# Kernel optimization log

Hardware: AMD Instinct MI355X
Metric: run time of the kernel (lower is better)

Reference implementation:

```python
import jax, jax.numpy as jnp
import numpy as np

N, C, G = 262144, 256, 1024
R = C // 4  # reduction bottleneck


def _linear_w(key, out_dim, in_dim):
    # torch.nn.Linear default init: U(-1/sqrt(in), 1/sqrt(in)), weight shape [out, in]
    bound = 1.0 / np.sqrt(in_dim)
    return jax.random.uniform(key, (out_dim, in_dim), jnp.float32, -bound, bound)


def setup_inputs() -> dict:
    key = jax.random.key(0)
    ks = jax.random.split(key, 8)
    return {
        "x": jax.random.normal(ks[0], (N, C), jnp.float32),
        "glb_w1": _linear_w(ks[1], R, C),
        "glb_a": jnp.full((1,), 0.25, jnp.float32),   # PReLU param (default init 0.25)
        "glb_w2": _linear_w(ks[2], C, R),
        "local_w1": _linear_w(ks[3], R, C),
        "local_a": jnp.full((1,), 0.25, jnp.float32),
        "local_w2": _linear_w(ks[4], C, R),
        "attn_w1": _linear_w(ks[5], R, C),
        "attn_a": jnp.full((1,), 0.25, jnp.float32),
        "attn_w2": _linear_w(ks[6], C, R),
        "batch_idx": jnp.sort(jax.random.randint(ks[7], (N,), 0, G)),
        "num_graphs": G,
    }


def _mlp(h, w1, a, w2):
    # Linear(no bias) -> PReLU -> Linear(no bias)
    z = jnp.einsum('nc,rc->nr', h, w1)
    z = jnp.where(z >= 0, z, a * z)
    return jnp.einsum('nr,cr->nc', z, w2)


def reference(x, glb_w1, glb_a, glb_w2, local_w1, local_a, local_w2,
              attn_w1, attn_a, attn_w2, batch_idx, num_graphs):
    g = _mlp(x, glb_w1, glb_a, glb_w2)                                  # [N, C]
    seg_sum = jax.ops.segment_sum(g, batch_idx, num_segments=num_graphs)  # [G, C]
    cnt = jax.ops.segment_sum(jnp.ones((x.shape[0], 1), x.dtype), batch_idx,
                              num_segments=num_graphs)                  # [G, 1]
    seg_mean = seg_sum / jnp.maximum(cnt, 1.0)  # scatter_mean (0 for empty graphs)
    x_glb = seg_mean[batch_idx]                                          # gather back [N, C]
    loc = _mlp(x, local_w1, local_a, local_w2)                           # [N, C]
    attn = _mlp(loc + x_glb, attn_w1, attn_a, attn_w2)
    return jax.nn.sigmoid(attn)
```

## Files before the change

kernel.cpp:

```cpp
#include <hip/hip_runtime.h>

typedef unsigned short u16;
typedef __attribute__((ext_vector_type(8))) short short8;
typedef __attribute__((ext_vector_type(4))) float f32x4;
typedef __attribute__((ext_vector_type(4))) unsigned short u16x4;
typedef __attribute__((ext_vector_type(2))) unsigned u32x2;

#define NN 262144
#define CC 256
#define RR 64
#define GG 1024

#define SWZ(b, n) ((b) ^ (((n) & 7) << 4))
#define SSWZ(b, r) ((b) ^ (((r) & 7) << 4))


static __device__ __forceinline__ u16 f2bf(float f) {
  unsigned u = __builtin_bit_cast(unsigned, f);
  u += 0x7fffu + ((u >> 16) & 1u);
  return (u16)(u >> 16);
}

static __device__ __forceinline__ unsigned cvt_pk_bf16(float lo, float hi) {
  unsigned r;
  asm("v_cvt_pk_bf16_f32 %0, %1, %2" : "=v"(r) : "v"(lo), "v"(hi));
  return r;
}

static __device__ __forceinline__ void lgkm0() {
  __asm__ volatile("s_waitcnt lgkmcnt(0)" ::: "memory");
}

#define MFMA16(a, b, c) __builtin_amdgcn_mfma_f32_16x16x32_bf16((a), (b), (c), 0, 0, 0)

__global__ void k_prep(const float* __restrict__ a0, const float* __restrict__ a1,
                       const float* __restrict__ a2, const float* __restrict__ a3,
                       const float* __restrict__ a4, const float* __restrict__ a5,
                       u16* __restrict__ dst, float* __restrict__ zbase) {
  int bid = blockIdx.x;
  if (bid < 96) {
    int m = bid >> 4;
    const float* s = (m == 0) ? a0 : (m == 1) ? a1 : (m == 2) ? a2
                   : (m == 3) ? a3 : (m == 4) ? a4 : a5;
    int off = (((bid & 15) << 8) | threadIdx.x) << 2;
    f32x4 v = *(const f32x4*)(s + off);
    u16x4 p;
    p[0] = f2bf(v[0]); p[1] = f2bf(v[1]); p[2] = f2bf(v[2]); p[3] = f2bf(v[3]);
    *(u16x4*)(dst + m * 16384 + off) = p;
  } else {
    int idx = (bid - 96) * 256 + threadIdx.x;
    ((f32x4*)zbase)[idx] = (f32x4){0.f, 0.f, 0.f, 0.f};
  }
}

#define ZBOFF 16384

__global__ __launch_bounds__(256)
__attribute__((amdgpu_waves_per_eu(8, 8))) void k_glb(
    const float* __restrict__ x, const u16* __restrict__ wbf,
    const int* __restrict__ bidx, const float* __restrict__ pa,
    float* __restrict__ seg, int* __restrict__ cnt) {
  __shared__ __align__(16) char smem[20480];
  const int tid = threadIdx.x;
  const int wave = tid >> 6, lane = tid & 63;
  const int low = lane & 15, quad = lane >> 4;
  const int node0 = blockIdx.x << 5;
  const float alpha = pa[0];
  const u16* w1 = wbf;
  const u16* w2 = wbf + 16384;

  const int lbv = bidx[node0 + (lane & 31)];

  const float* xsrc = x + (size_t)node0 * CC;
#pragma unroll
  for (int k = 0; k < 8; k++) {
    int f = k * 1024 + tid * 4;
    f32x4 v = *(const f32x4*)(xsrc + f);
    int node = f >> 8;
    u32x2 p;
    p[0] = cvt_pk_bf16(v[0], v[1]);
    p[1] = cvt_pk_bf16(v[2], v[3]);
    *(u32x2*)(smem + SWZ(node * 512 + (f & 255) * 2, node)) = p;
  }

  if (wave == 0) {
    int cur = __shfl(lbv, 0), rl = 0;
#pragma unroll
    for (int n = 0; n < 32; n++) {
      int b = __shfl(lbv, n);
      if (b != cur) { if (lane == 0) atomicAdd(cnt + cur, rl); rl = 0; cur = b; }
      rl++;
    }
    if (lane == 0) atomicAdd(cnt + cur, rl);
  }
  __syncthreads();

  f32x4 z[2] = {};
  const u16* w1p = w1 + (wave * 16 + low) * CC;
#pragma unroll
  for (int ks = 0; ks < 8; ks++) {
    short8 wa = *(const short8*)(w1p + ks * 32 + quad * 8);
#pragma unroll
    for (int nt = 0; nt < 2; nt++) {
      int node = nt * 16 + low;
      short8 xf = *(const short8*)(smem + SWZ(node * 512 + ks * 64 + quad * 16, node));
      z[nt] = MFMA16(wa, xf, z[nt]);
    }
  }
#pragma unroll
  for (int nt = 0; nt < 2; nt++) {
    float v0 = z[nt][0], v1 = z[nt][1], v2 = z[nt][2], v3 = z[nt][3];
    v0 = v0 >= 0.f ? v0 : alpha * v0;
    v1 = v1 >= 0.f ? v1 : alpha * v1;
    v2 = v2 >= 0.f ? v2 : alpha * v2;
    v3 = v3 >= 0.f ? v3 : alpha * v3;
    int node = nt * 16 + low;
    u32x2 p;
    p[0] = cvt_pk_bf16(v0, v1);
    p[1] = cvt_pk_bf16(v2, v3);
    *(u32x2*)(smem + ZBOFF + SWZ(node * 128 + wave * 32 + quad * 8, node)) = p;
  }
  __syncthreads();

  char* slab = smem + wave * 4096;
#pragma unroll
  for (int nt = 0; nt < 2; nt++) {
    int node = nt * 16 + low;
    f32x4 g[4] = {};
#pragma unroll
    for (int ks2 = 0; ks2 < 2; ks2++) {
      short8 zf = *(const short8*)(smem + ZBOFF + SWZ(node * 128 + ks2 * 64 + quad * 16, node));
#pragma unroll
      for (int mt = 0; mt < 4; mt++) {
        short8 wa = *(const short8*)(w2 + (wave * 64 + mt * 16 + low) * RR + ks2 * 32 + quad * 8);
        g[mt] = MFMA16(wa, zf, g[mt]);
      }
    }
#pragma unroll
    for (int mt = 0; mt < 4; mt++)
      *(f32x4*)(slab + SSWZ(low * 256 + mt * 64 + quad * 16, low)) = g[mt];
    lgkm0();
    float acc = 0.f;
    int cur = __shfl(lbv, nt * 16);
#pragma unroll
    for (int n = 0; n < 16; n++) {
      int b = __shfl(lbv, nt * 16 + n);
      if (b != cur) {
        atomicAdd(seg + (size_t)cur * CC + wave * 64 + lane, acc);
        acc = 0.f; cur = b;
      }
      acc += *(const float*)(slab + SSWZ(n * 256 + lane * 4, n));
    }
    atomicAdd(seg + (size_t)cur * CC + wave * 64 + lane, acc);
    lgkm0();
  }
}

__global__ __launch_bounds__(256)
__attribute__((amdgpu_waves_per_eu(8, 8))) void k_attn(
    const float* __restrict__ x, const u16* __restrict__ wbf,
    const int* __restrict__ bidx, const float* __restrict__ seg,
    const int* __restrict__ cnt,
    const float* __restrict__ pal, const float* __restrict__ paa,
    float* __restrict__ out) {
  __shared__ __align__(16) char smem[20480];
  const int tid = threadIdx.x;
  const int wave = tid >> 6, lane = tid & 63;
  const int low = lane & 15, quad = lane >> 4;
  const int node0 = blockIdx.x << 5;
  const float al = pal[0], aa = paa[0];
  const u16* w1l = wbf + 2 * 16384;
  const u16* w2l = wbf + 3 * 16384;
  const u16* w1a = wbf + 4 * 16384;
  const u16* w2a = wbf + 5 * 16384;

  int bb[2], cc[2];
#pragma unroll
  for (int nt = 0; nt < 2; nt++) bb[nt] = bidx[node0 + nt * 16 + low];
#pragma unroll
  for (int nt = 0; nt < 2; nt++) cc[nt] = cnt[bb[nt]];

  const float* xsrc = x + (size_t)node0 * CC;
#pragma unroll
  for (int k = 0; k < 8; k++) {
    int f = k * 1024 + tid * 4;
    f32x4 v = *(const f32x4*)(xsrc + f);
    int node = f >> 8;
    u32x2 p;
    p[0] = cvt_pk_bf16(v[0], v[1]);
    p[1] = cvt_pk_bf16(v[2], v[3]);
    *(u32x2*)(smem + SWZ(node * 512 + (f & 255) * 2, node)) = p;
  }
  __syncthreads();

  f32x4 z[2] = {};
  const u16* w1p = w1l + (wave * 16 + low) * CC;
#pragma unroll
  for (int ks = 0; ks < 8; ks++) {
    short8 wa = *(const short8*)(w1p + ks * 32 + quad * 8);
#pragma unroll
    for (int nt = 0; nt < 2; nt++) {
      int node = nt * 16 + low;
      short8 xf = *(const short8*)(smem + SWZ(node * 512 + ks * 64 + quad * 16, node));
      z[nt] = MFMA16(wa, xf, z[nt]);
    }
  }
#pragma unroll
  for (int nt = 0; nt < 2; nt++) {
    float v0 = z[nt][0], v1 = z[nt][1], v2 = z[nt][2], v3 = z[nt][3];
    v0 = v0 >= 0.f ? v0 : al * v0;
    v1 = v1 >= 0.f ? v1 : al * v1;
    v2 = v2 >= 0.f ? v2 : al * v2;
    v3 = v3 >= 0.f ? v3 : al * v3;
    int node = nt * 16 + low;
    u32x2 p;
    p[0] = cvt_pk_bf16(v0, v1);
    p[1] = cvt_pk_bf16(v2, v3);
    *(u32x2*)(smem + ZBOFF + SWZ(node * 128 + wave * 32 + quad * 8, node)) = p;
  }
  __syncthreads();

#pragma unroll
  for (int nt = 0; nt < 2; nt++) {
    int node = nt * 16 + low;
    f32x4 loc[4] = {};
#pragma unroll
    for (int ks2 = 0; ks2 < 2; ks2++) {
      short8 zf = *(const short8*)(smem + ZBOFF + SWZ(node * 128 + ks2 * 64 + quad * 16, node));
#pragma unroll
      for (int mt = 0; mt < 4; mt++) {
        short8 wa = *(const short8*)(w2l + (wave * 64 + mt * 16 + low) * RR + ks2 * 32 + quad * 8);
        loc[mt] = MFMA16(wa, zf, loc[mt]);
      }
    }
    const float* srow = seg + (size_t)bb[nt] * CC + wave * 64;
    float inv = (cc[nt] > 0) ? __builtin_amdgcn_rcpf((float)cc[nt]) : 0.0f;
#pragma unroll
    for (int mt = 0; mt < 4; mt++) {
      f32x4 sv = *(const f32x4*)(srow + mt * 16 + quad * 4);
      u32x2 p;
      p[0] = cvt_pk_bf16(fmaf(sv[0], inv, loc[mt][0]),
                         fmaf(sv[1], inv, loc[mt][1]));
      p[1] = cvt_pk_bf16(fmaf(sv[2], inv, loc[mt][2]),
                         fmaf(sv[3], inv, loc[mt][3]));
      *(u32x2*)(smem + SWZ(node * 512 + wave * 128 + mt * 32 + quad * 8, node)) = p;
    }
  }
  __syncthreads();

  f32x4 z2[2] = {};
  const u16* w1pa = w1a + (wave * 16 + low) * CC;
#pragma unroll
  for (int ks = 0; ks < 8; ks++) {
    short8 wa = *(const short8*)(w1pa + ks * 32 + quad * 8);
#pragma unroll
    for (int nt = 0; nt < 2; nt++) {
      int node = nt * 16 + low;
      short8 hf = *(const short8*)(smem + SWZ(node * 512 + ks * 64 + quad * 16, node));
      z2[nt] = MFMA16(wa, hf, z2[nt]);
    }
  }
#pragma unroll
  for (int nt = 0; nt < 2; nt++) {
    float v0 = z2[nt][0], v1 = z2[nt][1], v2 = z2[nt][2], v3 = z2[nt][3];
    v0 = v0 >= 0.f ? v0 : aa * v0;
    v1 = v1 >= 0.f ? v1 : aa * v1;
    v2 = v2 >= 0.f ? v2 : aa * v2;
    v3 = v3 >= 0.f ? v3 : aa * v3;
    int node = nt * 16 + low;
    u32x2 p;
    p[0] = cvt_pk_bf16(v0, v1);
    p[1] = cvt_pk_bf16(v2, v3);
    *(u32x2*)(smem + ZBOFF + SWZ(node * 128 + wave * 32 + quad * 8, node)) = p;
  }
  __syncthreads();

#pragma unroll
  for (int nt = 0; nt < 2; nt++) {
    int node = nt * 16 + low;
    f32x4 o[4] = {};
#pragma unroll
    for (int ks2 = 0; ks2 < 2; ks2++) {
      short8 zf = *(const short8*)(smem + ZBOFF + SWZ(node * 128 + ks2 * 64 + quad * 16, node));
#pragma unroll
      for (int mt = 0; mt < 4; mt++) {
        short8 wa = *(const short8*)(w2a + (wave * 64 + mt * 16 + low) * RR + ks2 * 32 + quad * 8);
        o[mt] = MFMA16(wa, zf, o[mt]);
      }
    }
    float* orow = out + (size_t)(node0 + node) * CC + wave * 64;
#pragma unroll
    for (int mt = 0; mt < 4; mt++) {
#pragma unroll
      for (int i = 0; i < 4; i++)
        o[mt][i] = __builtin_amdgcn_rcpf(1.0f + __expf(-o[mt][i]));
      *(f32x4*)(orow + mt * 16 + quad * 4) = o[mt];
    }
  }
}

extern "C" void kernel_launch(void* const* d_in, const int* in_sizes, int n_in,
                              void* d_out, int out_size, void* d_ws, size_t ws_size,
                              hipStream_t stream) {
  (void)in_sizes; (void)n_in; (void)out_size; (void)ws_size;
  const float* x   = (const float*)d_in[0];
  const float* w1g = (const float*)d_in[1];
  const float* ag  = (const float*)d_in[2];
  const float* w2g = (const float*)d_in[3];
  const float* w1l = (const float*)d_in[4];
  const float* al  = (const float*)d_in[5];
  const float* w2l = (const float*)d_in[6];
  const float* w1a = (const float*)d_in[7];
  const float* aa  = (const float*)d_in[8];
  const float* w2a = (const float*)d_in[9];
  const int* bidx  = (const int*)d_in[10];
  float* out = (float*)d_out;

  u16* wbf   = (u16*)d_ws;
  float* seg = (float*)((char*)d_ws + 196608);
  int* cnt   = (int*)((char*)d_ws + 196608 + 1048576);

  k_prep<<<353, 256, 0, stream>>>(w1g, w2g, w1l, w2l, w1a, w2a, wbf, seg);
  k_glb<<<NN / 32, 256, 0, stream>>>(x, wbf, bidx, ag, seg, cnt);
  k_attn<<<NN / 32, 256, 0, stream>>>(x, wbf, bidx, seg, cnt, al, aa, out);
}
```

Measured before the change: 683.8 us.

## Cache bf16-converted x tiles in workspace for reuse by attention kernel

The global-MLP kernel now also writes its swizzled bf16 copy of each x tile to a workspace buffer. When the workspace is large enough, the attention kernel loads that tile straight into LDS with global_load_lds instead of re-reading fp32 x and converting it. This halves the x read in the second kernel at the cost of an extra 128 MB write in the first. Occupancy hints on both kernels are lowered from 8 to 6 waves per EU.

```diff
diff --git a/kernel.cpp b/kernel.cpp
--- a/kernel.cpp
+++ b/kernel.cpp
@@ -14,6 +14,8 @@
 #define SWZ(b, n) ((b) ^ (((n) & 7) << 4))
 #define SSWZ(b, r) ((b) ^ (((r) & 7) << 4))
 
+#define XBFOFF 1249280
+#define XBFSZ  ((size_t)NN * CC * 2)
 
 static __device__ __forceinline__ u16 f2bf(float f) {
   unsigned u = __builtin_bit_cast(unsigned, f);
@@ -29,6 +31,12 @@
 
 static __device__ __forceinline__ void lgkm0() {
   __asm__ volatile("s_waitcnt lgkmcnt(0)" ::: "memory");
+}
+
+static __device__ __forceinline__ void gload_lds16(const void* g, void* l) {
+  __builtin_amdgcn_global_load_lds(
+      (const __attribute__((address_space(1))) void*)g,
+      (__attribute__((address_space(3))) void*)l, 16, 0, 0);
 }
 
 #define MFMA16(a, b, c) __builtin_amdgcn_mfma_f32_16x16x32_bf16((a), (b), (c), 0, 0, 0)
@@ -56,10 +64,11 @@
 #define ZBOFF 16384
 
 __global__ __launch_bounds__(256)
-__attribute__((amdgpu_waves_per_eu(8, 8))) void k_glb(
+__attribute__((amdgpu_waves_per_eu(6, 6))) void k_glb(
     const float* __restrict__ x, const u16* __restrict__ wbf,
     const int* __restrict__ bidx, const float* __restrict__ pa,
-    float* __restrict__ seg, int* __restrict__ cnt) {
+    float* __restrict__ seg, int* __restrict__ cnt,
+    char* __restrict__ xbf) {
   __shared__ __align__(16) char smem[20480];
   const int tid = threadIdx.x;
   const int wave = tid >> 6, lane = tid & 63;
@@ -72,6 +81,7 @@
   const int lbv = bidx[node0 + (lane & 31)];
 
   const float* xsrc = x + (size_t)node0 * CC;
+  char* xtile = xbf ? (xbf + ((size_t)blockIdx.x << 14)) : nullptr;
 #pragma unroll
   for (int k = 0; k < 8; k++) {
     int f = k * 1024 + tid * 4;
@@ -80,7 +90,9 @@
     u32x2 p;
     p[0] = cvt_pk_bf16(v[0], v[1]);
     p[1] = cvt_pk_bf16(v[2], v[3]);
-    *(u32x2*)(smem + SWZ(node * 512 + (f & 255) * 2, node)) = p;
+    int off = SWZ(node * 512 + (f & 255) * 2, node);
+    *(u32x2*)(smem + off) = p;
+    if (xtile) *(u32x2*)(xtile + off) = p;
   }
 
   if (wave == 0) {
@@ -156,9 +168,11 @@
   }
 }
 
+template <int USE_XBF>
 __global__ __launch_bounds__(256)
-__attribute__((amdgpu_waves_per_eu(8, 8))) void k_attn(
-    const float* __restrict__ x, const u16* __restrict__ wbf,
+__attribute__((amdgpu_waves_per_eu(6, 6))) void k_attn(
+    const float* __restrict__ x, const char* __restrict__ xbf,
+    const u16* __restrict__ wbf,
     const int* __restrict__ bidx, const float* __restrict__ seg,
     const int* __restrict__ cnt,
     const float* __restrict__ pal, const float* __restrict__ paa,
@@ -174,22 +188,32 @@
   const u16* w1a = wbf + 4 * 16384;
   const u16* w2a = wbf + 5 * 16384;
 
+  if (USE_XBF) {
+    const char* gsrc = xbf + ((size_t)blockIdx.x << 14) + wave * 1024 + lane * 16;
+    char* ldst = smem + wave * 1024 + lane * 16;
+#pragma unroll
+    for (int i = 0; i < 4; i++)
+      gload_lds16(gsrc + i * 4096, ldst + i * 4096);
+  }
+
   int bb[2], cc[2];
 #pragma unroll
   for (int nt = 0; nt < 2; nt++) bb[nt] = bidx[node0 + nt * 16 + low];
 #pragma unroll
   for (int nt = 0; nt < 2; nt++) cc[nt] = cnt[bb[nt]];
 
-  const float* xsrc = x + (size_t)node0 * CC;
-#pragma unroll
-  for (int k = 0; k < 8; k++) {
-    int f = k * 1024 + tid * 4;
-    f32x4 v = *(const f32x4*)(xsrc + f);
-    int node = f >> 8;
-    u32x2 p;
-    p[0] = cvt_pk_bf16(v[0], v[1]);
-    p[1] = cvt_pk_bf16(v[2], v[3]);
-    *(u32x2*)(smem + SWZ(node * 512 + (f & 255) * 2, node)) = p;
+  if (!USE_XBF) {
+    const float* xsrc = x + (size_t)node0 * CC;
+#pragma unroll
+    for (int k = 0; k < 8; k++) {
+      int f = k * 1024 + tid * 4;
+      f32x4 v = *(const f32x4*)(xsrc + f);
+      int node = f >> 8;
+      u32x2 p;
+      p[0] = cvt_pk_bf16(v[0], v[1]);
+      p[1] = cvt_pk_bf16(v[2], v[3]);
+      *(u32x2*)(smem + SWZ(node * 512 + (f & 255) * 2, node)) = p;
+    }
   }
   __syncthreads();
 
@@ -302,7 +326,7 @@
 extern "C" void kernel_launch(void* const* d_in, const int* in_sizes, int n_in,
                               void* d_out, int out_size, void* d_ws, size_t ws_size,
                               hipStream_t stream) {
-  (void)in_sizes; (void)n_in; (void)out_size; (void)ws_size;
+  (void)in_sizes; (void)n_in; (void)out_size;
   const float* x   = (const float*)d_in[0];
   const float* w1g = (const float*)d_in[1];
   const float* ag  = (const float*)d_in[2];
@@ -319,8 +343,13 @@
   u16* wbf   = (u16*)d_ws;
   float* seg = (float*)((char*)d_ws + 196608);
   int* cnt   = (int*)((char*)d_ws + 196608 + 1048576);
+  const bool big = ws_size >= (size_t)XBFOFF + XBFSZ;
+  char* xbf  = big ? ((char*)d_ws + XBFOFF) : nullptr;
 
   k_prep<<<353, 256, 0, stream>>>(w1g, w2g, w1l, w2l, w1a, w2a, wbf, seg);
-  k_glb<<<NN / 32, 256, 0, stream>>>(x, wbf, bidx, ag, seg, cnt);
-  k_attn<<<NN / 32, 256, 0, stream>>>(x, wbf, bidx, seg, cnt, al, aa, out);
-}
+  k_glb<<<NN / 32, 256, 0, stream>>>(x, wbf, bidx, ag, seg, cnt, xbf);
+  if (big)
+    k_attn<1><<<NN / 32, 256, 0, stream>>>(x, xbf, wbf, bidx, seg, cnt, al, aa, out);
+  else
+    k_attn<0><<<NN / 32, 256, 0, stream>>>(x, xbf, wbf, bidx, seg, cnt, al, aa, out);
+}
```

Result: no change. 679.3 us (-0.6%).
